# Optimization experiments

Measured on AMD Instinct MI355X. Metric: run time of the kernel, lower is better.

Reference implementation:

```python
import jax, jax.numpy as jnp
import numpy as np

D = 1024; H = 16; HD = D // H; E = 8; K = 2; F = 4096; L = 2; R = 3; V = 8192; B = 256; S = 512
EPS = 1e-5

def _ln(x, g, b):
    m = x.mean(-1, keepdims=True)
    v = ((x - m) ** 2).mean(-1, keepdims=True)
    return (x - m) * jax.lax.rsqrt(v + EPS) * g + b

def _attn(q, k, v, wq, bq, wk, bk, wv, bv, wo, bo, causal):
    Bq, Tq, _ = q.shape; Tk = k.shape[1]
    Q = (q @ wq + bq).reshape(Bq, Tq, H, HD).transpose(0, 2, 1, 3)
    Kk = (k @ wk + bk).reshape(Bq, Tk, H, HD).transpose(0, 2, 1, 3)
    Vv = (v @ wv + bv).reshape(Bq, Tk, H, HD).transpose(0, 2, 1, 3)
    s = jnp.einsum('bhqd,bhkd->bhqk', Q, Kk) / np.sqrt(HD).astype(np.float32)
    if causal:
        mask = jnp.tril(jnp.ones((Tq, Tk), dtype=bool))
        s = jnp.where(mask, s, -jnp.inf)
    a = jax.nn.softmax(s, axis=-1)
    o = jnp.einsum('bhqk,bhkd->bhqd', a, Vv).transpose(0, 2, 1, 3).reshape(Bq, Tq, D)
    return o @ wo + bo

def _moe(x, rw, rb, w1, b1, w2, b2):
    # x: [T, D]. Dense-per-expert compute + one-hot combine == masked gather/scatter in original.
    probs = jax.nn.softmax(x @ rw + rb, axis=-1)            # [T, E]
    tw, ti = jax.lax.top_k(probs, K)                        # [T, K]
    tw = jax.nn.softmax(tw, axis=-1)
    gate = (jax.nn.one_hot(ti, E, dtype=x.dtype) * tw[..., None]).sum(1)  # [T, E]
    h = jax.nn.gelu(jnp.einsum('td,edf->etf', x, w1) + b1[:, None, :], approximate=False)
    y = jnp.einsum('etf,efd->etd', h, w2) + b2[:, None, :]  # [E, T, D]
    return jnp.einsum('etd,te->td', y, gate)

def setup_inputs() -> dict:
    key = jax.random.key(0)
    ks = iter(jax.random.split(key, 64))
    n = lambda shape, s=0.02: jax.random.normal(next(ks), shape, dtype=jnp.float32) * s
    inp = {
        'semantic_ids': jax.random.randint(next(ks), (B, R), 0, V, dtype=jnp.int32),
        'encoder_output': jax.random.normal(next(ks), (B, S, D), dtype=jnp.float32),
        'emb_tables': n((R, V, D)), 'bos_emb': n((D,)),
        'sa_wq': n((L, D, D)), 'sa_bq': jnp.zeros((L, D)), 'sa_wk': n((L, D, D)), 'sa_bk': jnp.zeros((L, D)),
        'sa_wv': n((L, D, D)), 'sa_bv': jnp.zeros((L, D)), 'sa_wo': n((L, D, D)), 'sa_bo': jnp.zeros((L, D)),
        'ca_wq': n((L, D, D)), 'ca_bq': jnp.zeros((L, D)), 'ca_wk': n((L, D, D)), 'ca_bk': jnp.zeros((L, D)),
        'ca_wv': n((L, D, D)), 'ca_bv': jnp.zeros((L, D)), 'ca_wo': n((L, D, D)), 'ca_bo': jnp.zeros((L, D)),
        'router_w': n((L, D, E)), 'router_b': jnp.zeros((L, E)),
        'moe_w1': n((L, E, D, F)), 'moe_b1': jnp.zeros((L, E, F)),
        'moe_w2': n((L, E, F, D)), 'moe_b2': jnp.zeros((L, E, D)),
        'ln1_g': jnp.ones((L, D)), 'ln1_b': jnp.zeros((L, D)),
        'ln2_g': jnp.ones((L, D)), 'ln2_b': jnp.zeros((L, D)),
        'ln3_g': jnp.ones((L, D)), 'ln3_b': jnp.zeros((L, D)),
        'lnf_g': jnp.ones((D,)), 'lnf_b': jnp.zeros((D,)),
        'out_w': n((R, D, V)), 'out_b': jnp.zeros((R, V)),
    }
    return inp

def reference(semantic_ids, encoder_output, emb_tables, bos_emb,
              sa_wq, sa_bq, sa_wk, sa_bk, sa_wv, sa_bv, sa_wo, sa_bo,
              ca_wq, ca_bq, ca_wk, ca_bk, ca_wv, ca_bv, ca_wo, ca_bo,
              router_w, router_b, moe_w1, moe_b1, moe_w2, moe_b2,
              ln1_g, ln1_b, ln2_g, ln2_b, ln3_g, ln3_b, lnf_g, lnf_b, out_w, out_b):
    Bsz = semantic_ids.shape[0]
    emb = emb_tables[jnp.arange(R), semantic_ids]                  # [B, R, D]
    bos = jnp.broadcast_to(bos_emb, (Bsz, 1, D))
    x = jnp.concatenate([bos, emb], axis=1)                        # [B, R+1, D]
    T = x.shape[1]
    for i in range(L):
        x = _ln(x + _attn(x, x, x, sa_wq[i], sa_bq[i], sa_wk[i], sa_bk[i], sa_wv[i], sa_bv[i], sa_wo[i], sa_bo[i], True), ln1_g[i], ln1_b[i])
        x = _ln(x + _attn(x, encoder_output, encoder_output, ca_wq[i], ca_bq[i], ca_wk[i], ca_bk[i], ca_wv[i], ca_bv[i], ca_wo[i], ca_bo[i], False), ln2_g[i], ln2_b[i])
        moe_out = _moe(x.reshape(-1, D), router_w[i], router_b[i], moe_w1[i], moe_b1[i], moe_w2[i], moe_b2[i]).reshape(Bsz, T, D)
        x = _ln(x + moe_out, ln3_g[i], ln3_b[i])
    x = _ln(x, lnf_g, lnf_b)
    logits = jnp.einsum('brd,rdv->brv', x[:, :R, :], out_w) + out_b  # positions 0..R-1
    return logits
```

## Files before the change

kernel.cpp:

```cpp
#include <hip/hip_runtime.h>
#include <math.h>

typedef __attribute__((ext_vector_type(4))) float f32x4;
typedef __attribute__((ext_vector_type(8))) short s16x8;

__device__ __forceinline__ unsigned short f2bf(float f){
  union { float f; unsigned u; } v; v.f = f;
  return (unsigned short)((v.u + 0x7fffu + ((v.u >> 16) & 1u)) >> 16);
}
__device__ __forceinline__ float bf2f(unsigned short h){
  union { unsigned u; float f; } v; v.u = ((unsigned)h) << 16;
  return v.f;
}
struct HL { short hi, lo; };
__device__ __forceinline__ HL split2(float v){
  union { float f; unsigned u; } c; c.f = v;
  unsigned short h = (unsigned short)(c.u >> 16);
  HL r; r.hi = (short)h; r.lo = (short)f2bf(v - bf2f(h));
  return r;
}

template<int BM, int BN, bool BT, int EPI, bool QKV3>
__global__ __launch_bounds__(256)
void gemm_k(const float* __restrict__ Ap, const float* __restrict__ Bp,
            const float* __restrict__ Bp1, const float* __restrict__ Bp2,
            const float* __restrict__ bias, const float* __restrict__ bias1,
            const float* __restrict__ bias2,
            const float* __restrict__ resid, float* __restrict__ Cp,
            int K, int ldb, int ldc,
            int rdiv, long rs1, long rs2, long zsa, long zsb, long zsc, int zbias,
            float alpha, const int* __restrict__ rowlim, int kspl, long zscs)
{
  const int z = blockIdx.z;
  const int e = z / kspl, sps = z - e*kspl;
  const long kbeg = (long)sps * K;
  if (rowlim && (long)blockIdx.y * BM >= (long)rowlim[e]) return;

  const float* Bsel = Bp; const float* bsel = bias;
  if constexpr (QKV3){
    if (e == 1){ Bsel = Bp1; bsel = bias1; }
    else if (e == 2){ Bsel = Bp2; bsel = bias2; }
  }

  constexpr int NGA = BM/64;
  constexpr int NGB = BN/64;
  constexpr int LOG2BN = (BN == 128 ? 7 : 6);

  __shared__ short As[2][BM*32];
  __shared__ short Bs[2][BN*32];

  const int tid  = threadIdx.x;
  const int lane = tid & 63;
  const int wid  = tid >> 6;
  const int wr   = wid >> 1, wc = wid & 1;
  constexpr int WM = BM/2, WN = BN/2;
  constexpr int MR = WM/16, NR = WN/16;

  const long blockM = (long)blockIdx.y * BM;
  const long blockN = (long)blockIdx.x * BN;

  long aoffG[NGA]; int aoffL[NGA];
#pragma unroll
  for (int i = 0; i < NGA; ++i){
    int g = i*256 + tid;
    int row = g >> 2, kg = g & 3;
    long gm = blockM + row;
    aoffG[i] = (gm / rdiv) * rs1 + (gm % rdiv) * rs2 + (long)e * zsa + kbeg + kg*8;
    aoffL[i] = (row >> 4)*512 + kg*128 + (row & 15)*8;
  }
  long boffG[NGB]; int boffL[NGB]; int bkg[NGB];
#pragma unroll
  for (int i = 0; i < NGB; ++i){
    int g = i*256 + tid;
    if constexpr (BT){
      int row = g >> 2, kg = g & 3;
      boffG[i] = (long)e * zsb + (blockN + row) * (long)ldb + kbeg + kg*8;
      boffL[i] = (row >> 4)*512 + kg*128 + (row & 15)*8;
      bkg[i] = 0;
    } else {
      int n = g & (BN-1), kg = g >> LOG2BN;
      boffG[i] = (long)e * zsb + blockN + n;
      bkg[i] = kg;
      boffL[i] = (n >> 4)*512 + kg*128 + (n & 15)*8;
    }
  }

  f32x4 acc[MR][NR];
#pragma unroll
  for (int m = 0; m < MR; ++m)
#pragma unroll
    for (int n = 0; n < NR; ++n)
      acc[m][n] = (f32x4){0.f, 0.f, 0.f, 0.f};

  const int lrow = lane & 15;
  const int kg   = lane >> 4;

  auto loadA = [&](int kk, f32x4 (*a)[2]){
#pragma unroll
    for (int i = 0; i < NGA; ++i){
      a[i][0] = *(const f32x4*)(Ap + aoffG[i] + kk);
      a[i][1] = *(const f32x4*)(Ap + aoffG[i] + kk + 4);
    }
  };
  auto loadB = [&](int kk, f32x4 (*b)[2]){
#pragma unroll
    for (int i = 0; i < NGB; ++i){
      if constexpr (BT){
        b[i][0] = *(const f32x4*)(Bsel + boffG[i] + kk);
        b[i][1] = *(const f32x4*)(Bsel + boffG[i] + kk + 4);
      } else {
        long kb = kbeg + kk + bkg[i]*8;
#pragma unroll
        for (int j = 0; j < 4; ++j){
          b[i][0][j] = Bsel[boffG[i] + (kb + j)     * (long)ldb];
          b[i][1][j] = Bsel[boffG[i] + (kb + 4 + j) * (long)ldb];
        }
      }
    }
  };
  auto mk8 = [&](const f32x4& v0, const f32x4& v1, s16x8& hi, s16x8& lo){
    HL h;
    h = split2(v0.x); hi[0]=h.hi; lo[0]=h.lo;
    h = split2(v0.y); hi[1]=h.hi; lo[1]=h.lo;
    h = split2(v0.z); hi[2]=h.hi; lo[2]=h.lo;
    h = split2(v0.w); hi[3]=h.hi; lo[3]=h.lo;
    h = split2(v1.x); hi[4]=h.hi; lo[4]=h.lo;
    h = split2(v1.y); hi[5]=h.hi; lo[5]=h.lo;
    h = split2(v1.z); hi[6]=h.hi; lo[6]=h.lo;
    h = split2(v1.w); hi[7]=h.hi; lo[7]=h.lo;
  };
  auto process = [&](f32x4 (*a)[2], f32x4 (*b)[2]){
    __syncthreads();
#pragma unroll
    for (int i = 0; i < NGA; ++i){
      s16x8 hi, lo; mk8(a[i][0], a[i][1], hi, lo);
      *(s16x8*)&As[0][aoffL[i]] = hi;
      *(s16x8*)&As[1][aoffL[i]] = lo;
    }
#pragma unroll
    for (int i = 0; i < NGB; ++i){
      s16x8 hi, lo; mk8(b[i][0], b[i][1], hi, lo);
      *(s16x8*)&Bs[0][boffL[i]] = hi;
      *(s16x8*)&Bs[1][boffL[i]] = lo;
    }
    __syncthreads();

    s16x8 afh[MR], afl[MR], bfh[NR], bfl[NR];
#pragma unroll
    for (int m = 0; m < MR; ++m){
      int off = (wr*MR + m)*512 + kg*128 + lrow*8;
      afh[m] = *(const s16x8*)&As[0][off];
      afl[m] = *(const s16x8*)&As[1][off];
    }
#pragma unroll
    for (int n = 0; n < NR; ++n){
      int off = (wc*NR + n)*512 + kg*128 + lrow*8;
      bfh[n] = *(const s16x8*)&Bs[0][off];
      bfl[n] = *(const s16x8*)&Bs[1][off];
    }
#pragma unroll
    for (int m = 0; m < MR; ++m)
#pragma unroll
      for (int n = 0; n < NR; ++n){
        acc[m][n] = __builtin_amdgcn_mfma_f32_16x16x32_bf16(afh[m], bfh[n], acc[m][n], 0, 0, 0);
        acc[m][n] = __builtin_amdgcn_mfma_f32_16x16x32_bf16(afl[m], bfh[n], acc[m][n], 0, 0, 0);
        acc[m][n] = __builtin_amdgcn_mfma_f32_16x16x32_bf16(afh[m], bfl[n], acc[m][n], 0, 0, 0);
      }
  };

  f32x4 a0[NGA][2], a1[NGA][2], b0[NGB][2], b1[NGB][2];
  loadA(0, a0); loadB(0, b0);
  for (int k0 = 0; k0 < K; k0 += 64){
    loadA(k0 + 32, a1); loadB(k0 + 32, b1);
    process(a0, b0);
    if (k0 + 64 < K){ loadA(k0 + 64, a0); loadB(k0 + 64, b0); }
    process(a1, b1);
  }

#pragma unroll
  for (int n = 0; n < NR; ++n){
    long gn = blockN + wc*WN + n*16 + lrow;
    float bv = 0.f;
    if constexpr ((EPI & 1) != 0) bv = bsel[(long)e * zbias + gn];
#pragma unroll
    for (int m = 0; m < MR; ++m){
#pragma unroll
      for (int j = 0; j < 4; ++j){
        long gm = blockM + wr*WM + m*16 + kg*4 + j;
        long cidx = (long)e * zsc + sps * zscs + gm * (long)ldc + gn;
        float v = acc[m][n][j] * alpha + bv;
        if constexpr ((EPI & 2) != 0) v += resid[cidx];
        if constexpr ((EPI & 4) != 0) v = 0.5f * v * (1.0f + erff(v * 0.70710678f));
        Cp[cidx] = v;
      }
    }
  }
}

__global__ __launch_bounds__(256)
void embed_k(const int* __restrict__ ids, const float* __restrict__ embt,
             const float* __restrict__ bos, float* __restrict__ x)
{
  int t = blockIdx.x;
  int b = t >> 2, q = t & 3;
  const float* src;
  if (q == 0) src = bos;
  else {
    int r = q - 1;
    long id = ids[b*3 + r];
    src = embt + ((long)r * 8192 + id) * 1024;
  }
  f32x4 v = *(const f32x4*)(src + threadIdx.x * 4);
  *(f32x4*)(x + (long)t * 1024 + threadIdx.x * 4) = v;
}

__global__ __launch_bounds__(64)
void sattn_k(const float* __restrict__ Q, const float* __restrict__ Kk,
             const float* __restrict__ V, float* __restrict__ O)
{
  int tid = blockIdx.x * 64 + threadIdx.x;
  int q = tid & 3, h = (tid >> 2) & 15;
  long b = tid >> 6;
  long t = b*4 + q;
  const float* qp = Q + t*1024 + h*64;
  float s[4]; float mx = -1e30f;
  for (int k = 0; k <= q; ++k){
    const float* kp = Kk + (b*4 + k)*1024 + h*64;
    float a = 0.f;
#pragma unroll
    for (int d = 0; d < 64; ++d) a += qp[d] * kp[d];
    s[k] = a * 0.125f; mx = fmaxf(mx, s[k]);
  }
  float den = 0.f;
  for (int k = 0; k <= q; ++k){ s[k] = expf(s[k] - mx); den += s[k]; }
  float inv = 1.f / den;
  float* op = O + t*1024 + h*64;
  for (int d = 0; d < 64; ++d){
    float a = 0.f;
    for (int k = 0; k <= q; ++k) a += s[k] * V[(b*4 + k)*1024 + h*64 + d];
    op[d] = a * inv;
  }
}

__global__ __launch_bounds__(256)
void ln_k(const float* __restrict__ in, const float* __restrict__ g,
          const float* __restrict__ b, float* __restrict__ out)
{
  __shared__ float red[8];
  long row = blockIdx.x;
  int tid = threadIdx.x, lane = tid & 63, wid = tid >> 6;
  f32x4 v = ((const f32x4*)(in + row*1024))[tid];
  float s  = v.x + v.y + v.z + v.w;
  float s2 = v.x*v.x + v.y*v.y + v.z*v.z + v.w*v.w;
  for (int o = 32; o; o >>= 1){ s += __shfl_down(s, o); s2 += __shfl_down(s2, o); }
  if (!lane){ red[wid] = s; red[4 + wid] = s2; }
  __syncthreads();
  if (tid == 0){
    float S = red[0]+red[1]+red[2]+red[3], S2 = red[4]+red[5]+red[6]+red[7];
    float m = S * (1.f/1024.f);
    float var = S2 * (1.f/1024.f) - m*m;
    red[0] = m; red[1] = 1.0f / sqrtf(var + 1e-5f);
  }
  __syncthreads();
  float m = red[0], r = red[1];
  f32x4 gv = ((const f32x4*)g)[tid], bv = ((const f32x4*)b)[tid];
  f32x4 o;
  o.x = (v.x - m)*r*gv.x + bv.x; o.y = (v.y - m)*r*gv.y + bv.y;
  o.z = (v.z - m)*r*gv.z + bv.z; o.w = (v.w - m)*r*gv.w + bv.w;
  ((f32x4*)(out + row*1024))[tid] = o;
}

__global__ __launch_bounds__(256)
void moe_ln_k(const float* __restrict__ x, const float* __restrict__ Yg4,
              const float* __restrict__ gwp, const int* __restrict__ sg,
              const float* __restrict__ b2,
              const float* __restrict__ g, const float* __restrict__ b,
              float* __restrict__ out)
{
  __shared__ float red[8];
  long t = blockIdx.x;
  int tid = threadIdx.x, lane = tid & 63, wid = tid >> 6;
  float w0 = gwp[t*2], w1 = gwp[t*2 + 1];
  long r0 = sg[t*2], r1 = sg[t*2 + 1];
  long e0 = r0 >> 10, e1 = r1 >> 10;
  const long SP = 8388608;
  f32x4 y0 = ((const f32x4*)(Yg4 + 0*SP + r0*1024))[tid];
  f32x4 y1 = ((const f32x4*)(Yg4 + 0*SP + r1*1024))[tid];
#pragma unroll
  for (int s = 1; s < 4; ++s){
    y0 = y0 + ((const f32x4*)(Yg4 + s*SP + r0*1024))[tid];
    y1 = y1 + ((const f32x4*)(Yg4 + s*SP + r1*1024))[tid];
  }
  y0 = y0 + ((const f32x4*)(b2 + e0*1024))[tid];
  y1 = y1 + ((const f32x4*)(b2 + e1*1024))[tid];
  f32x4 v = ((const f32x4*)(x + t*1024))[tid];
  v = v + y0*w0 + y1*w1;
  float s  = v.x + v.y + v.z + v.w;
  float s2 = v.x*v.x + v.y*v.y + v.z*v.z + v.w*v.w;
  for (int o = 32; o; o >>= 1){ s += __shfl_down(s, o); s2 += __shfl_down(s2, o); }
  if (!lane){ red[wid] = s; red[4 + wid] = s2; }
  __syncthreads();
  if (tid == 0){
    float S = red[0]+red[1]+red[2]+red[3], S2 = red[4]+red[5]+red[6]+red[7];
    float m = S * (1.f/1024.f);
    float var = S2 * (1.f/1024.f) - m*m;
    red[0] = m; red[1] = 1.0f / sqrtf(var + 1e-5f);
  }
  __syncthreads();
  float m = red[0], r = red[1];
  f32x4 gv = ((const f32x4*)g)[tid], bv = ((const f32x4*)b)[tid];
  f32x4 o;
  o.x = (v.x - m)*r*gv.x + bv.x; o.y = (v.y - m)*r*gv.y + bv.y;
  o.z = (v.z - m)*r*gv.z + bv.z; o.w = (v.w - m)*r*gv.w + bv.w;
  ((f32x4*)(out + t*1024))[tid] = o;
}

__global__ __launch_bounds__(64)
void router_gather_k(const float* __restrict__ x, const float* __restrict__ rw,
                     const float* __restrict__ rb, int* __restrict__ cnt,
                     float* __restrict__ gw, int* __restrict__ sg,
                     float* __restrict__ xg)
{
  long t = blockIdx.x;
  int lane = threadIdx.x;
  __shared__ int ssl[2];
  float acc[8] = {0,0,0,0,0,0,0,0};
  const float* xp = x + t*1024;
  for (int i = 0; i < 16; ++i){
    float xv = xp[lane + i*64];
    const float* w = rw + (long)(lane + i*64) * 8;
#pragma unroll
    for (int e = 0; e < 8; ++e) acc[e] += xv * w[e];
  }
#pragma unroll
  for (int e = 0; e < 8; ++e)
    for (int o = 32; o; o >>= 1) acc[e] += __shfl_down(acc[e], o);
  if (lane == 0){
    float l[8]; float mx = -1e30f;
#pragma unroll
    for (int e = 0; e < 8; ++e){ l[e] = acc[e] + rb[e]; mx = fmaxf(mx, l[e]); }
    float ssum = 0.f;
#pragma unroll
    for (int e = 0; e < 8; ++e){ l[e] = expf(l[e] - mx); ssum += l[e]; }
    float inv = 1.f / ssum;
#pragma unroll
    for (int e = 0; e < 8; ++e) l[e] *= inv;
    int i0 = 0; float p0 = l[0];
#pragma unroll
    for (int e = 1; e < 8; ++e) if (l[e] > p0){ p0 = l[e]; i0 = e; }
    int i1 = -1; float p1 = -1e30f;
#pragma unroll
    for (int e = 0; e < 8; ++e) if (e != i0 && l[e] > p1){ p1 = l[e]; i1 = e; }
    float w0 = 1.f / (1.f + expf(p1 - p0));
    int s0 = atomicAdd(&cnt[i0], 1);
    int s1 = atomicAdd(&cnt[i1], 1);
    int r0 = i0*1024 + s0, r1 = i1*1024 + s1;
    gw[t*2] = w0; gw[t*2 + 1] = 1.f - w0;
    sg[t*2] = r0; sg[t*2 + 1] = r1;
    ssl[0] = r0; ssl[1] = r1;
  }
  __syncthreads();
  const f32x4* xp4 = (const f32x4*)(x + t*1024);
#pragma unroll
  for (int r = 0; r < 2; ++r){
    f32x4* dp = (f32x4*)(xg + (long)ssl[r]*1024);
#pragma unroll
    for (int i = 0; i < 4; ++i) dp[lane + i*64] = xp4[lane + i*64];
  }
}

__global__ __launch_bounds__(256)
void casm_k(float* __restrict__ S)
{
  long row = (long)blockIdx.x * 4 + (threadIdx.x >> 6);
  int lane = threadIdx.x & 63;
  float* p = S + row * 512;
  f32x4 a = *(const f32x4*)(p + lane*4);
  f32x4 c = *(const f32x4*)(p + 256 + lane*4);
  float mx = fmaxf(fmaxf(fmaxf(a.x, a.y), fmaxf(a.z, a.w)),
                   fmaxf(fmaxf(c.x, c.y), fmaxf(c.z, c.w)));
  for (int o = 32; o; o >>= 1) mx = fmaxf(mx, __shfl_xor(mx, o));
  a.x = expf(a.x - mx); a.y = expf(a.y - mx); a.z = expf(a.z - mx); a.w = expf(a.w - mx);
  c.x = expf(c.x - mx); c.y = expf(c.y - mx); c.z = expf(c.z - mx); c.w = expf(c.w - mx);
  float sm = a.x+a.y+a.z+a.w + c.x+c.y+c.z+c.w;
  for (int o = 32; o; o >>= 1) sm += __shfl_xor(sm, o);
  float inv = 1.f / sm;
  *(f32x4*)(p + lane*4) = a * inv;
  *(f32x4*)(p + 256 + lane*4) = c * inv;
}

extern "C" void kernel_launch(void* const* d_in, const int* in_sizes, int n_in,
                              void* d_out, int out_size, void* d_ws, size_t ws_size,
                              hipStream_t stream)
{
  (void)in_sizes; (void)n_in; (void)out_size; (void)ws_size;
  const int*   sem  = (const int*)  d_in[0];
  const float* enc  = (const float*)d_in[1];
  const float* embt = (const float*)d_in[2];
  const float* bos  = (const float*)d_in[3];
  const float* sa_wq = (const float*)d_in[4];  const float* sa_bq = (const float*)d_in[5];
  const float* sa_wk = (const float*)d_in[6];  const float* sa_bk = (const float*)d_in[7];
  const float* sa_wv = (const float*)d_in[8];  const float* sa_bv = (const float*)d_in[9];
  const float* sa_wo = (const float*)d_in[10]; const float* sa_bo = (const float*)d_in[11];
  const float* ca_wq = (const float*)d_in[12]; const float* ca_bq = (const float*)d_in[13];
  const float* ca_wk = (const float*)d_in[14];
  const float* ca_wv = (const float*)d_in[16]; const float* ca_bv = (const float*)d_in[17];
  const float* ca_wo = (const float*)d_in[18]; const float* ca_bo = (const float*)d_in[19];
  const float* rw_   = (const float*)d_in[20]; const float* rb_   = (const float*)d_in[21];
  const float* w1_   = (const float*)d_in[22]; const float* b1_   = (const float*)d_in[23];
  const float* w2_   = (const float*)d_in[24]; const float* b2_   = (const float*)d_in[25];
  const float* ln1g = (const float*)d_in[26];  const float* ln1b = (const float*)d_in[27];
  const float* ln2g = (const float*)d_in[28];  const float* ln2b = (const float*)d_in[29];
  const float* ln3g = (const float*)d_in[30];  const float* ln3b = (const float*)d_in[31];
  const float* lnfg = (const float*)d_in[32];  const float* lnfb = (const float*)d_in[33];
  const float* outw = (const float*)d_in[34];  const float* outb = (const float*)d_in[35];
  float* logits = (float*)d_out;

  float* ws = (float*)d_ws;
  const long M1 = 1l << 20;
  float* x   = ws;
  float* Qb  = ws + 1*M1;
  float* Kb  = ws + 2*M1;
  float* Vb  = ws + 3*M1;
  float* Ob  = ws + 4*M1;
  float* tmp = ws + 5*M1;
  float* gw  = ws + 6*M1;
  int*   cnt = (int*)(ws + 6*M1 + 4096);
  int*   sg  = (int*)(ws + 6*M1 + 4352);
  float* big = ws + 6*M1 + 8192;
  float* Aca = big;
  float* S   = big + 16*M1;
  float* Op  = big;
  float* xg  = big;
  float* Hg  = big + 8*M1;
  float* Yg4 = big + 40*M1;

  embed_k<<<dim3(1024), dim3(256), 0, stream>>>(sem, embt, bos, x);

  for (int i = 0; i < 2; ++i){
    const long iM = (long)i * 1048576;
    const float *wq = sa_wq + iM, *bq = sa_bq + i*1024;
    const float *wk = sa_wk + iM, *bk = sa_bk + i*1024;
    const float *wv = sa_wv + iM, *bv = sa_bv + i*1024;
    const float *wo = sa_wo + iM, *bo = sa_bo + i*1024;
    const float *cq = ca_wq + iM, *cbq = ca_bq + i*1024;
    const float *cwk = ca_wk + iM;
    const float *cwv = ca_wv + iM, *cbv = ca_bv + i*1024;
    const float *cwo = ca_wo + iM, *cbo = ca_bo + i*1024;
    const float *rw = rw_ + (long)i*8192, *rb = rb_ + i*8;
    const float *w1 = w1_ + (long)i*33554432, *b1 = b1_ + (long)i*32768;
    const float *w2 = w2_ + (long)i*33554432, *b2 = b2_ + (long)i*8192;

    gemm_k<64,64,false,1,true><<<dim3(16,16,3),dim3(256),0,stream>>>(
        x, wq, wk, wv, bq, bk, bv, nullptr, Qb,
        1024,1024,1024, 1,1024,0, 0,0,1048576, 0, 1.0f, nullptr, 1, 0);
    sattn_k<<<dim3(256),dim3(64),0,stream>>>(Qb, Kb, Vb, Ob);
    gemm_k<64,64,false,3,false><<<dim3(16,16,1),dim3(256),0,stream>>>(
        Ob, wo, nullptr,nullptr, bo, nullptr,nullptr, x, tmp,
        1024,1024,1024, 1,1024,0, 0,0,0, 0, 1.0f, nullptr, 1, 0);
    ln_k<<<dim3(1024),dim3(256),0,stream>>>(tmp, ln1g + i*1024, ln1b + i*1024, x);

    gemm_k<64,64,false,1,false><<<dim3(16,16,1),dim3(256),0,stream>>>(
        x, cq, nullptr,nullptr, cbq, nullptr,nullptr, nullptr, Qb,
        1024,1024,1024, 1,1024,0, 0,0,0, 0, 1.0f, nullptr, 1, 0);
    gemm_k<128,128,true,0,false><<<dim3(8,8,16),dim3(256),0,stream>>>(
        Qb, cwk, nullptr,nullptr, nullptr, nullptr,nullptr, nullptr, Aca,
        64,1024,1024, 1,1024,0, 64,64,1048576, 0, 0.125f, nullptr, 1, 0);
    gemm_k<64,128,true,0,false><<<dim3(4,1,256),dim3(256),0,stream>>>(
        Aca, enc, nullptr,nullptr, nullptr, nullptr,nullptr, nullptr, S,
        1024,1024,512, 4,1048576,1024, 4096,524288,32768, 0, 1.0f, nullptr, 1, 0);
    casm_k<<<dim3(4096),dim3(256),0,stream>>>(S);
    gemm_k<64,128,false,0,false><<<dim3(8,1,256),dim3(256),0,stream>>>(
        S, enc, nullptr,nullptr, nullptr, nullptr,nullptr, nullptr, Op,
        512,1024,1024, 1,512,0, 32768,524288,65536, 0, 1.0f, nullptr, 1, 0);
    gemm_k<64,64,false,1,false><<<dim3(1,16,16),dim3(256),0,stream>>>(
        Op, cwv, nullptr,nullptr, cbv, nullptr,nullptr, nullptr, Ob,
        1024,1024,1024, 4,65536,1024, 4096,64,64, 64, 1.0f, nullptr, 1, 0);
    gemm_k<64,64,false,3,false><<<dim3(16,16,1),dim3(256),0,stream>>>(
        Ob, cwo, nullptr,nullptr, cbo, nullptr,nullptr, x, tmp,
        1024,1024,1024, 1,1024,0, 0,0,0, 0, 1.0f, nullptr, 1, 0);
    ln_k<<<dim3(1024),dim3(256),0,stream>>>(tmp, ln2g + i*1024, ln2b + i*1024, x);

    (void)hipMemsetAsync(cnt, 0, 8*sizeof(int), stream);
    router_gather_k<<<dim3(1024),dim3(64),0,stream>>>(x, rw, rb, cnt, gw, sg, xg);
    gemm_k<128,128,false,5,false><<<dim3(32,8,8),dim3(256),0,stream>>>(
        xg, w1, nullptr,nullptr, b1, nullptr,nullptr, nullptr, Hg,
        1024,4096,4096, 1,1024,0, 1048576,4194304,4194304, 4096, 1.0f, cnt, 1, 0);
    gemm_k<128,128,false,0,false><<<dim3(8,8,32),dim3(256),0,stream>>>(
        Hg, w2, nullptr,nullptr, nullptr, nullptr,nullptr, nullptr, Yg4,
        1024,1024,1024, 1,4096,0, 4194304,4194304,1048576, 0, 1.0f, cnt, 4, 8388608);
    moe_ln_k<<<dim3(1024),dim3(256),0,stream>>>(x, Yg4, gw, sg, b2,
                                                ln3g + i*1024, ln3b + i*1024, x);
  }

  ln_k<<<dim3(1024),dim3(256),0,stream>>>(x, lnfg, lnfb, tmp);
  gemm_k<128,128,false,1,false><<<dim3(64,2,3),dim3(256),0,stream>>>(
      tmp, outw, nullptr,nullptr, outb, nullptr,nullptr, nullptr, logits,
      1024,8192,24576, 1,4096,0, 1024,8388608,8192, 8192, 1.0f, nullptr, 1, 0);
}
```

Measured before the change: 1.970 ms.

## Fuse cross-attention scores, softmax and PV into a flash-style kernel

```diff
diff --git a/kernel.cpp b/kernel.cpp
--- a/kernel.cpp
+++ b/kernel.cpp
@@ -18,6 +18,17 @@
   unsigned short h = (unsigned short)(c.u >> 16);
   HL r; r.hi = (short)h; r.lo = (short)f2bf(v - bf2f(h));
   return r;
+}
+__device__ __forceinline__ void mk8(const f32x4& v0, const f32x4& v1, s16x8& hi, s16x8& lo){
+  HL h;
+  h = split2(v0.x); hi[0]=h.hi; lo[0]=h.lo;
+  h = split2(v0.y); hi[1]=h.hi; lo[1]=h.lo;
+  h = split2(v0.z); hi[2]=h.hi; lo[2]=h.lo;
+  h = split2(v0.w); hi[3]=h.hi; lo[3]=h.lo;
+  h = split2(v1.x); hi[4]=h.hi; lo[4]=h.lo;
+  h = split2(v1.y); hi[5]=h.hi; lo[5]=h.lo;
+  h = split2(v1.z); hi[6]=h.hi; lo[6]=h.lo;
+  h = split2(v1.w); hi[7]=h.hi; lo[7]=h.lo;
 }
 
 template<int BM, int BN, bool BT, int EPI, bool QKV3>
@@ -118,17 +129,6 @@
       }
     }
   };
-  auto mk8 = [&](const f32x4& v0, const f32x4& v1, s16x8& hi, s16x8& lo){
-    HL h;
-    h = split2(v0.x); hi[0]=h.hi; lo[0]=h.lo;
-    h = split2(v0.y); hi[1]=h.hi; lo[1]=h.lo;
-    h = split2(v0.z); hi[2]=h.hi; lo[2]=h.lo;
-    h = split2(v0.w); hi[3]=h.hi; lo[3]=h.lo;
-    h = split2(v1.x); hi[4]=h.hi; lo[4]=h.lo;
-    h = split2(v1.y); hi[5]=h.hi; lo[5]=h.lo;
-    h = split2(v1.z); hi[6]=h.hi; lo[6]=h.lo;
-    h = split2(v1.w); hi[7]=h.hi; lo[7]=h.lo;
-  };
   auto process = [&](f32x4 (*a)[2], f32x4 (*b)[2]){
     __syncthreads();
 #pragma unroll
@@ -191,10 +191,171 @@
         float v = acc[m][n][j] * alpha + bv;
         if constexpr ((EPI & 2) != 0) v += resid[cidx];
         if constexpr ((EPI & 4) != 0) v = 0.5f * v * (1.0f + erff(v * 0.70710678f));
-        Cp[cidx] = v;
-      }
-    }
-  }
+        if constexpr ((EPI & 8) != 0){
+          HL s = split2(v);
+          ((unsigned short*)Cp)[cidx] = (unsigned short)s.hi;
+          ((unsigned short*)Cp)[cidx + zscs] = (unsigned short)s.lo;
+        } else {
+          Cp[cidx] = v;
+        }
+      }
+    }
+  }
+}
+
+__global__ __launch_bounds__(512)
+void cattn_k(const unsigned short* __restrict__ AH, const unsigned short* __restrict__ AL,
+             const float* __restrict__ enc, float* __restrict__ Op)
+{
+  __shared__ short EH[2][16384];
+  __shared__ short EL[2][16384];
+  __shared__ short PHs[1024];
+  __shared__ short PLs[1024];
+  __shared__ float mrun[64], lrun[64], scl[64];
+
+  const int tid = threadIdx.x;
+  const int l   = tid & 63;
+  const int w   = tid >> 6;
+  const long b  = blockIdx.x;
+
+  f32x4 acc[4][8];
+#pragma unroll
+  for (int rt = 0; rt < 4; ++rt)
+#pragma unroll
+    for (int nt = 0; nt < 8; ++nt)
+      acc[rt][nt] = (f32x4){0.f,0.f,0.f,0.f};
+
+  if (tid < 64){ mrun[tid] = -3.0e38f; lrun[tid] = 0.0f; }
+
+  long qoff = 0;
+  if (w < 4){
+    int row = w*16 + (l & 15);
+    qoff = ((long)(row >> 2) * 1024 + b*4 + (row & 3)) * 1024 + (l >> 4)*8;
+  }
+
+  auto stage = [&](int chunk, int sbuf){
+    int u = tid - 256;
+    int key = u >> 4;
+    int d8  = (u & 15) * 8;
+    const float* src = enc + ((long)b*512 + chunk*16 + key)*1024 + d8;
+    int offb = (key>>2)*4096 + (key&3)*16 + (d8 & 15);
+    int dsb  = d8 >> 4;
+#pragma unroll
+    for (int j = 0; j < 8; ++j){
+      f32x4 v0 = *(const f32x4*)(src + j*128);
+      f32x4 v1 = *(const f32x4*)(src + j*128 + 4);
+      s16x8 hi, lo; mk8(v0, v1, hi, lo);
+      int off = offb + (dsb + j*8)*64;
+      *(s16x8*)&EH[sbuf][off] = hi;
+      *(s16x8*)&EL[sbuf][off] = lo;
+    }
+  };
+
+  if (w >= 4) stage(0, 0);
+  __syncthreads();
+
+  for (int c = 0; c < 32; ++c){
+    const int buf = c & 1;
+    if (w < 4){
+      f32x4 s = (f32x4){0.f,0.f,0.f,0.f};
+      const int key = l & 15;
+      const int offb = (key>>2)*4096 + (key&3)*16 + (((l>>4)&1)*8);
+      const int dsb = (l>>4) >> 1;
+#pragma unroll 4
+      for (int ks = 0; ks < 32; ++ks){
+        s16x8 ah = *(const s16x8*)(AH + qoff + ks*32);
+        s16x8 al = *(const s16x8*)(AL + qoff + ks*32);
+        int off = offb + (ks*2 + dsb)*64;
+        s16x8 bh = *(const s16x8*)&EH[buf][off];
+        s16x8 bl = *(const s16x8*)&EL[buf][off];
+        s = __builtin_amdgcn_mfma_f32_16x16x32_bf16(ah, bh, s, 0, 0, 0);
+        s = __builtin_amdgcn_mfma_f32_16x16x32_bf16(al, bh, s, 0, 0, 0);
+        s = __builtin_amdgcn_mfma_f32_16x16x32_bf16(ah, bl, s, 0, 0, 0);
+      }
+#pragma unroll
+      for (int j = 0; j < 4; ++j){
+        float mx = s[j];
+        for (int o = 1; o < 16; o <<= 1) mx = fmaxf(mx, __shfl_xor(mx, o));
+        int row = w*16 + (l>>4)*4 + j;
+        float mo = mrun[row];
+        float mn = fmaxf(mo, mx);
+        float sc = expf(mo - mn);
+        float p  = expf(s[j] - mn);
+        float ps = p;
+        for (int o = 1; o < 16; o <<= 1) ps += __shfl_xor(ps, o);
+        if ((l & 15) == 0){
+          mrun[row] = mn; scl[row] = sc;
+          lrun[row] = lrun[row]*sc + ps;
+        }
+        HL hp = split2(p);
+        PHs[row*16 + key] = hp.hi;
+        PLs[row*16 + key] = hp.lo;
+      }
+    } else {
+      if (c + 1 < 32) stage(c + 1, buf ^ 1);
+    }
+    __syncthreads();
+
+#pragma unroll
+    for (int rt = 0; rt < 4; ++rt)
+#pragma unroll
+      for (int j = 0; j < 4; ++j){
+        float sv = scl[rt*16 + (l>>4)*4 + j];
+#pragma unroll
+        for (int nt = 0; nt < 8; ++nt) acc[rt][nt][j] *= sv;
+      }
+
+    s16x8 pfh[4], pfl[4];
+    {
+      const int kb = ((l>>4)&1)*8;
+#pragma unroll
+      for (int rt = 0; rt < 4; ++rt){
+        int row = rt*16 + (l & 15);
+        s16x8 ph = *(const s16x8*)&PHs[row*16 + kb];
+        s16x8 pl = *(const s16x8*)&PLs[row*16 + kb];
+        if (l >= 32){
+#pragma unroll
+          for (int i = 0; i < 8; ++i){ ph[i] = 0; pl[i] = 0; }
+        }
+        pfh[rt] = ph; pfl[rt] = pl;
+      }
+    }
+    {
+      const int kg2 = ((l>>4)&1)*8;
+#pragma unroll
+      for (int nt = 0; nt < 8; ++nt){
+        int dn = w*8 + nt;
+        s16x8 bh, bl;
+#pragma unroll
+        for (int j = 0; j < 8; ++j){
+          int key = kg2 + j;
+          int off = (key>>2)*4096 + dn*64 + (key&3)*16 + (l & 15);
+          bh[j] = EH[buf][off];
+          bl[j] = EL[buf][off];
+        }
+#pragma unroll
+        for (int rt = 0; rt < 4; ++rt){
+          acc[rt][nt] = __builtin_amdgcn_mfma_f32_16x16x32_bf16(pfh[rt], bh, acc[rt][nt], 0, 0, 0);
+          acc[rt][nt] = __builtin_amdgcn_mfma_f32_16x16x32_bf16(pfl[rt], bh, acc[rt][nt], 0, 0, 0);
+          acc[rt][nt] = __builtin_amdgcn_mfma_f32_16x16x32_bf16(pfh[rt], bl, acc[rt][nt], 0, 0, 0);
+        }
+      }
+    }
+    __syncthreads();
+  }
+
+#pragma unroll
+  for (int rt = 0; rt < 4; ++rt)
+#pragma unroll
+    for (int j = 0; j < 4; ++j){
+      int row = rt*16 + (l>>4)*4 + j;
+      float inv = 1.0f / lrun[row];
+#pragma unroll
+      for (int nt = 0; nt < 8; ++nt){
+        long cidx = (b*64 + row)*1024 + w*128 + nt*16 + (l & 15);
+        Op[cidx] = acc[rt][nt][j] * inv;
+      }
+    }
 }
 
 __global__ __launch_bounds__(256)
@@ -336,21 +497,21 @@
   for (int e = 0; e < 8; ++e)
     for (int o = 32; o; o >>= 1) acc[e] += __shfl_down(acc[e], o);
   if (lane == 0){
-    float l[8]; float mx = -1e30f;
-#pragma unroll
-    for (int e = 0; e < 8; ++e){ l[e] = acc[e] + rb[e]; mx = fmaxf(mx, l[e]); }
+    float lg[8]; float mx = -1e30f;
+#pragma unroll
+    for (int e = 0; e < 8; ++e){ lg[e] = acc[e] + rb[e]; mx = fmaxf(mx, lg[e]); }
     float ssum = 0.f;
 #pragma unroll
-    for (int e = 0; e < 8; ++e){ l[e] = expf(l[e] - mx); ssum += l[e]; }
+    for (int e = 0; e < 8; ++e){ lg[e] = expf(lg[e] - mx); ssum += lg[e]; }
     float inv = 1.f / ssum;
 #pragma unroll
-    for (int e = 0; e < 8; ++e) l[e] *= inv;
-    int i0 = 0; float p0 = l[0];
-#pragma unroll
-    for (int e = 1; e < 8; ++e) if (l[e] > p0){ p0 = l[e]; i0 = e; }
+    for (int e = 0; e < 8; ++e) lg[e] *= inv;
+    int i0 = 0; float p0 = lg[0];
+#pragma unroll
+    for (int e = 1; e < 8; ++e) if (lg[e] > p0){ p0 = lg[e]; i0 = e; }
     int i1 = -1; float p1 = -1e30f;
 #pragma unroll
-    for (int e = 0; e < 8; ++e) if (e != i0 && l[e] > p1){ p1 = l[e]; i1 = e; }
+    for (int e = 0; e < 8; ++e) if (e != i0 && lg[e] > p1){ p1 = lg[e]; i1 = e; }
     float w0 = 1.f / (1.f + expf(p1 - p0));
     int s0 = atomicAdd(&cnt[i0], 1);
     int s1 = atomicAdd(&cnt[i1], 1);
@@ -367,26 +528,6 @@
 #pragma unroll
     for (int i = 0; i < 4; ++i) dp[lane + i*64] = xp4[lane + i*64];
   }
-}
-
-__global__ __launch_bounds__(256)
-void casm_k(float* __restrict__ S)
-{
-  long row = (long)blockIdx.x * 4 + (threadIdx.x >> 6);
-  int lane = threadIdx.x & 63;
-  float* p = S + row * 512;
-  f32x4 a = *(const f32x4*)(p + lane*4);
-  f32x4 c = *(const f32x4*)(p + 256 + lane*4);
-  float mx = fmaxf(fmaxf(fmaxf(a.x, a.y), fmaxf(a.z, a.w)),
-                   fmaxf(fmaxf(c.x, c.y), fmaxf(c.z, c.w)));
-  for (int o = 32; o; o >>= 1) mx = fmaxf(mx, __shfl_xor(mx, o));
-  a.x = expf(a.x - mx); a.y = expf(a.y - mx); a.z = expf(a.z - mx); a.w = expf(a.w - mx);
-  c.x = expf(c.x - mx); c.y = expf(c.y - mx); c.z = expf(c.z - mx); c.w = expf(c.w - mx);
-  float sm = a.x+a.y+a.z+a.w + c.x+c.y+c.z+c.w;
-  for (int o = 32; o; o >>= 1) sm += __shfl_xor(sm, o);
-  float inv = 1.f / sm;
-  *(f32x4*)(p + lane*4) = a * inv;
-  *(f32x4*)(p + 256 + lane*4) = c * inv;
 }
 
 extern "C" void kernel_launch(void* const* d_in, const int* in_sizes, int n_in,
@@ -428,9 +569,8 @@
   int*   cnt = (int*)(ws + 6*M1 + 4096);
   int*   sg  = (int*)(ws + 6*M1 + 4352);
   float* big = ws + 6*M1 + 8192;
-  float* Aca = big;
-  float* S   = big + 16*M1;
-  float* Op  = big;
+  unsigned short* AcaH = (unsigned short*)big;
+  float* Op  = big + 16*M1;
   float* xg  = big;
   float* Hg  = big + 8*M1;
   float* Yg4 = big + 40*M1;
@@ -463,16 +603,10 @@
     gemm_k<64,64,false,1,false><<<dim3(16,16,1),dim3(256),0,stream>>>(
         x, cq, nullptr,nullptr, cbq, nullptr,nullptr, nullptr, Qb,
         1024,1024,1024, 1,1024,0, 0,0,0, 0, 1.0f, nullptr, 1, 0);
-    gemm_k<128,128,true,0,false><<<dim3(8,8,16),dim3(256),0,stream>>>(
-        Qb, cwk, nullptr,nullptr, nullptr, nullptr,nullptr, nullptr, Aca,
-        64,1024,1024, 1,1024,0, 64,64,1048576, 0, 0.125f, nullptr, 1, 0);
-    gemm_k<64,128,true,0,false><<<dim3(4,1,256),dim3(256),0,stream>>>(
-        Aca, enc, nullptr,nullptr, nullptr, nullptr,nullptr, nullptr, S,
-        1024,1024,512, 4,1048576,1024, 4096,524288,32768, 0, 1.0f, nullptr, 1, 0);
-    casm_k<<<dim3(4096),dim3(256),0,stream>>>(S);
-    gemm_k<64,128,false,0,false><<<dim3(8,1,256),dim3(256),0,stream>>>(
-        S, enc, nullptr,nullptr, nullptr, nullptr,nullptr, nullptr, Op,
-        512,1024,1024, 1,512,0, 32768,524288,65536, 0, 1.0f, nullptr, 1, 0);
+    gemm_k<128,128,true,8,false><<<dim3(8,8,16),dim3(256),0,stream>>>(
+        Qb, cwk, nullptr,nullptr, nullptr, nullptr,nullptr, nullptr, (float*)AcaH,
+        64,1024,1024, 1,1024,0, 64,64,1048576, 0, 0.125f, nullptr, 1, 16777216);
+    cattn_k<<<dim3(256),dim3(512),0,stream>>>(AcaH, AcaH + 16777216, enc, Op);
     gemm_k<64,64,false,1,false><<<dim3(1,16,16),dim3(256),0,stream>>>(
         Op, cwv, nullptr,nullptr, cbv, nullptr,nullptr, nullptr, Ob,
         1024,1024,1024, 4,65536,1024, 4096,64,64, 64, 1.0f, nullptr, 1, 0);
```

Result: slower. 2.378 ms (+20.7%).
